# Kernel optimization log

Hardware: AMD Instinct MI355X
Metric: run time of the kernel (lower is better)

The kernel has to match this reference:

```python
import jax, jax.numpy as jnp
import numpy as np


def setup_inputs() -> dict:
    key = jax.random.key(0)
    ks = jax.random.split(key, 5)
    n, raw, d, h = 1024, 128, 128, 256
    s = lambda fan: 1.0 / np.sqrt(fan)
    return {
        "x": jax.random.normal(ks[0], (n, raw), jnp.float32),
        "W_enc": jax.random.normal(ks[1], (raw, d), jnp.float32) * s(raw),
        "b_enc": jnp.zeros((d,), jnp.float32),
        "W1": jax.random.normal(ks[2], (2 * d, h), jnp.float32) * s(2 * d),
        "b1": jnp.zeros((h,), jnp.float32),
        "W2": jax.random.normal(ks[3], (h, 1), jnp.float32) * s(h),
        "b2": jnp.zeros((1,), jnp.float32),
    }


def reference(x, W_enc, b_enc, W1, b1, W2, b2):
    # pathVAE.encode stand-in: linear projection to latent mean
    z = x @ W_enc + b_enc                      # [n, d]
    n, d = z.shape
    # Original builds feat[i, j] = concat(z[j], z[i]) of shape [n*n, 2d],
    # then Linear(2d->h). Split W1 so the quadratic concat is never built:
    # h[i, j] = z[j] @ W1[:d] + z[i] @ W1[d:] + b1
    A = z @ W1[:d]                             # acts on the "a" (j) half
    B = z @ W1[d:]                             # acts on the "b" (i) half
    hmat = A[None, :, :] + B[:, None, :] + b1  # [n, n, h]
    hmat = jax.nn.selu(hmat)
    o = hmat @ W2 + b2                         # [n, n, 1]
    o = jax.nn.hard_sigmoid(o)                 # relu6(x+3)/6, same as torch
    return o.reshape(n, n)
```

## Files before the change

### kernel.cpp

```cpp
#include <hip/hip_runtime.h>
#include <math.h>


#define LOG2E       1.4426950408889634f
#define SELU_AS     1.7580993408473766f
#define S_OVER_L2E  0.7282921587620419f

typedef float v2f __attribute__((ext_vector_type(2)));

__global__ __launch_bounds__(256) void prep_kernel(
    const float* __restrict__ x, const float* __restrict__ W_enc,
    const float* __restrict__ b_enc, const float* __restrict__ W1,
    const float* __restrict__ b1, const float* __restrict__ W2,
    const float* __restrict__ b2, float* __restrict__ PAI,
    float* __restrict__ PBI, float* __restrict__ basep)
{
    __shared__ float zs[512];
    int t = threadIdx.x, b = blockIdx.x;
    if (b < 256) {
        int r0 = b << 2;
        int r = t >> 6;
        int dd = (t & 63) << 1;
        const float* xr = x + (size_t)(r0 + r) * 128;
        v2f z = { b_enc[dd], b_enc[dd + 1] };
#pragma unroll 8
        for (int dl = 0; dl < 128; ++dl) {
            float xv = xr[dl];
            v2f xx = { xv, xv };
            v2f wv = *(const v2f*)(W_enc + (size_t)dl * 128 + dd);
            z = __builtin_elementwise_fma(xx, wv, z);
        }
        zs[r * 128 + dd] = z.x;
        zs[r * 128 + dd + 1] = z.y;
        __syncthreads();

        int c = t;
        float b1c = b1[c];
        float accA0 = 0.f, accA1 = 0.f, accA2 = 0.f, accA3 = 0.f;
        float accB0 = b1c, accB1 = b1c, accB2 = b1c, accB3 = b1c;
        const float* w1a = W1 + c;
        const float* w1b = W1 + 128 * 256 + c;
#pragma unroll 4
        for (int dl = 0; dl < 128; ++dl) {
            float wa = w1a[(size_t)dl * 256];
            float wb = w1b[(size_t)dl * 256];
            float z0 = zs[dl], z1 = zs[128 + dl], z2 = zs[256 + dl], z3 = zs[384 + dl];
            accA0 = fmaf(z0, wa, accA0); accB0 = fmaf(z0, wb, accB0);
            accA1 = fmaf(z1, wa, accA1); accB1 = fmaf(z1, wb, accB1);
            accA2 = fmaf(z2, wa, accA2); accB2 = fmaf(z2, wb, accB2);
            accA3 = fmaf(z3, wa, accA3); accB3 = fmaf(z3, wb, accB3);
        }
        float a0 = accA0 * LOG2E, a1 = accA1 * LOG2E;
        float a2 = accA2 * LOG2E, a3 = accA3 * LOG2E;
        float bb0 = accB0 * LOG2E, bb1 = accB1 * LOG2E;
        float bb2v = accB2 * LOG2E, bb3 = accB3 * LOG2E;
        float4 pa0, pa1, pb0, pb1;
        pa0.x = a0; pa0.y = a1;
        pa0.z = __builtin_amdgcn_exp2f(a0); pa0.w = __builtin_amdgcn_exp2f(a1);
        pa1.x = a2; pa1.y = a3;
        pa1.z = __builtin_amdgcn_exp2f(a2); pa1.w = __builtin_amdgcn_exp2f(a3);
        pb0.x = bb0; pb0.y = bb1;
        pb0.z = __builtin_amdgcn_exp2f(bb0); pb0.w = __builtin_amdgcn_exp2f(bb1);
        pb1.x = bb2v; pb1.y = bb3;
        pb1.z = __builtin_amdgcn_exp2f(bb2v); pb1.w = __builtin_amdgcn_exp2f(bb3);
        size_t o = (size_t)c * 2048 + (size_t)(r0 << 1);
        *(float4*)(PAI + o) = pa0;
        *(float4*)(PAI + o + 4) = pa1;
        *(float4*)(PBI + o) = pb0;
        *(float4*)(PBI + o + 4) = pb1;
    } else if (t < 64) {
        float s = W2[t] + W2[t + 64] + W2[t + 128] + W2[t + 192];
#pragma unroll
        for (int o = 32; o > 0; o >>= 1) s += __shfl_down(s, o);
        if (t == 0) basep[0] = fmaf(-SELU_AS, s, b2[0]);
    }
}

__global__ __launch_bounds__(256, 4) void pair_kernel(
    const float* __restrict__ PAI, const float* __restrict__ PBI,
    const float* __restrict__ W2, const float* __restrict__ basep,
    float* __restrict__ out)
{
    __shared__ __align__(16) float As[64 * 64];
    __shared__ __align__(16) float Bs[64 * 64];

    int t = threadIdx.x;
    int bj32 = blockIdx.x << 5, bi32 = blockIdx.y << 5;
    int jp = t & 15;
    int ip = t >> 4;

    v2f acc1[2] = {{0.f, 0.f}, {0.f, 0.f}};
    v2f acc2[2] = {{0.f, 0.f}, {0.f, 0.f}};
    const v2f vzero = {0.f, 0.f};
    const v2f vone  = {1.f, 1.f};

    for (int kc = 0; kc < 4; ++kc) {
        int k0 = kc << 6;
        if (kc) __syncthreads();
#pragma unroll
        for (int p = 0; p < 4; ++p) {
            int f = (p << 8) + t;
            int k_l = f >> 4;
            int col = (f & 15) << 2;
            size_t go = (size_t)(k0 + k_l) * 2048;
            *(float4*)&As[f << 2] = *(const float4*)(PAI + go + (bj32 << 1) + col);
            *(float4*)&Bs[f << 2] = *(const float4*)(PBI + go + (bi32 << 1) + col);
        }
        __syncthreads();

        const float* W2c = W2 + k0;
#pragma unroll 8
        for (int k = 0; k < 64; ++k) {
            float w = W2c[k];
            float4 av = *(const float4*)&As[(k << 6) + (jp << 2)];
            float4 bv = *(const float4*)&Bs[(k << 6) + (ip << 2)];
            v2f a01 = { av.x, av.y }, e01 = { av.z, av.w };
            v2f wv = { w, w };
#pragma unroll
            for (int i = 0; i < 2; ++i) {
                float bi = i ? bv.y : bv.x;
                float ei = i ? bv.w : bv.z;
                v2f bbv = { bi, bi };
                v2f eev = { ei, ei };
                v2f t01 = a01 + bbv;
                v2f p01 = e01 * eev;
                t01 = __builtin_elementwise_max(t01, vzero);
                p01 = __builtin_elementwise_min(p01, vone);
                acc1[i] = __builtin_elementwise_fma(wv, t01, acc1[i]);
                acc2[i] = __builtin_elementwise_fma(wv, p01, acc2[i]);
            }
        }
    }

    float base = basep[0];
    v2f basev = { base, base };
    v2f c1 = { S_OVER_L2E, S_OVER_L2E };
    v2f c2 = { SELU_AS, SELU_AS };
#pragma unroll
    for (int i = 0; i < 2; ++i) {
        v2f v = __builtin_elementwise_fma(c1, acc1[i],
                __builtin_elementwise_fma(c2, acc2[i], basev));
        float2 o;
        o.x = __saturatef(v.x * (1.0f / 6.0f) + 0.5f);
        o.y = __saturatef(v.y * (1.0f / 6.0f) + 0.5f);
        *(float2*)(out + (size_t)(bi32 + (ip << 1) + i) * 1024
                       + bj32 + (jp << 1)) = o;
    }
}

extern "C" void kernel_launch(void* const* d_in, const int* in_sizes, int n_in,
                              void* d_out, int out_size, void* d_ws, size_t ws_size,
                              hipStream_t stream) {
    const float* x     = (const float*)d_in[0];
    const float* W_enc = (const float*)d_in[1];
    const float* b_enc = (const float*)d_in[2];
    const float* W1    = (const float*)d_in[3];
    const float* b1    = (const float*)d_in[4];
    const float* W2    = (const float*)d_in[5];
    const float* b2    = (const float*)d_in[6];
    float* out = (float*)d_out;

    float* ws = (float*)d_ws;
    const int PLANE = 256 * 2048;
    float* PAI = ws;
    float* PBI = ws + PLANE;
    float* basep = ws + 2 * PLANE;

    prep_kernel<<<257, 256, 0, stream>>>(x, W_enc, b_enc, W1, b1, W2, b2,
                                         PAI, PBI, basep);
    pair_kernel<<<dim3(32, 32), 256, 0, stream>>>(PAI, PBI, W2, basep, out);
}
```

Baseline: 127.7 us.

## Use packed fp16 pair math with fdot2 and a larger 4x4 register tile

The prep kernel now stores the A/B projections and their exponentials as packed half2 values, with pairs of hidden units interleaved through lane shuffles. It also converts W2 to half2. The pair kernel computes add/max and mul/min in packed fp16 and accumulates with v_dot2 into fp32. Each thread now computes a 4x4 output tile over a 64x64 block instead of 2x2 over 32x32, which raises register reuse of the LDS loads. This roughly halves the ALU work per hidden unit, at the cost of fp16 precision for exp values and activations, which may overflow or lose accuracy.

```diff
diff --git a/kernel.cpp b/kernel.cpp
--- a/kernel.cpp
+++ b/kernel.cpp
@@ -7,13 +7,16 @@
 #define S_OVER_L2E  0.7282921587620419f
 
 typedef float v2f __attribute__((ext_vector_type(2)));
+typedef _Float16 v2h __attribute__((ext_vector_type(2)));
+typedef unsigned int u32;
 
 __global__ __launch_bounds__(256) void prep_kernel(
     const float* __restrict__ x, const float* __restrict__ W_enc,
     const float* __restrict__ b_enc, const float* __restrict__ W1,
     const float* __restrict__ b1, const float* __restrict__ W2,
-    const float* __restrict__ b2, float* __restrict__ PAI,
-    float* __restrict__ PBI, float* __restrict__ basep)
+    const float* __restrict__ b2, u32* __restrict__ PAa,
+    u32* __restrict__ PAe, u32* __restrict__ PBb, u32* __restrict__ PBe,
+    u32* __restrict__ W2h, float* __restrict__ basep)
 {
     __shared__ float zs[512];
     int t = threadIdx.x, b = blockIdx.x;
@@ -50,101 +53,129 @@
             accA2 = fmaf(z2, wa, accA2); accB2 = fmaf(z2, wb, accB2);
             accA3 = fmaf(z3, wa, accA3); accB3 = fmaf(z3, wb, accB3);
         }
-        float a0 = accA0 * LOG2E, a1 = accA1 * LOG2E;
-        float a2 = accA2 * LOG2E, a3 = accA3 * LOG2E;
-        float bb0 = accB0 * LOG2E, bb1 = accB1 * LOG2E;
-        float bb2v = accB2 * LOG2E, bb3 = accB3 * LOG2E;
-        float4 pa0, pa1, pb0, pb1;
-        pa0.x = a0; pa0.y = a1;
-        pa0.z = __builtin_amdgcn_exp2f(a0); pa0.w = __builtin_amdgcn_exp2f(a1);
-        pa1.x = a2; pa1.y = a3;
-        pa1.z = __builtin_amdgcn_exp2f(a2); pa1.w = __builtin_amdgcn_exp2f(a3);
-        pb0.x = bb0; pb0.y = bb1;
-        pb0.z = __builtin_amdgcn_exp2f(bb0); pb0.w = __builtin_amdgcn_exp2f(bb1);
-        pb1.x = bb2v; pb1.y = bb3;
-        pb1.z = __builtin_amdgcn_exp2f(bb2v); pb1.w = __builtin_amdgcn_exp2f(bb3);
-        size_t o = (size_t)c * 2048 + (size_t)(r0 << 1);
-        *(float4*)(PAI + o) = pa0;
-        *(float4*)(PAI + o + 4) = pa1;
-        *(float4*)(PBI + o) = pb0;
-        *(float4*)(PBI + o + 4) = pb1;
-    } else if (t < 64) {
-        float s = W2[t] + W2[t + 64] + W2[t + 128] + W2[t + 192];
-#pragma unroll
-        for (int o = 32; o > 0; o >>= 1) s += __shfl_down(s, o);
-        if (t == 0) basep[0] = fmaf(-SELU_AS, s, b2[0]);
+        float ar[4] = { accA0 * LOG2E, accA1 * LOG2E, accA2 * LOG2E, accA3 * LOG2E };
+        float br[4] = { accB0 * LOG2E, accB1 * LOG2E, accB2 * LOG2E, accB3 * LOG2E };
+        u32 pa[4], pe[4], pb[4], pf[4];
+        bool odd = (c & 1);
+#pragma unroll
+        for (int r2 = 0; r2 < 4; ++r2) {
+            float er = __builtin_amdgcn_exp2f(ar[r2]);
+            float fr = __builtin_amdgcn_exp2f(br[r2]);
+            float aN = __shfl_xor(ar[r2], 1);
+            float eN = __shfl_xor(er, 1);
+            float bN = __shfl_xor(br[r2], 1);
+            float fN = __shfl_xor(fr, 1);
+            pa[r2] = __builtin_bit_cast(u32, __builtin_amdgcn_cvt_pkrtz(ar[r2], aN));
+            pe[r2] = __builtin_bit_cast(u32, __builtin_amdgcn_cvt_pkrtz(er, eN));
+            pb[r2] = __builtin_bit_cast(u32, __builtin_amdgcn_cvt_pkrtz(bN, br[r2]));
+            pf[r2] = __builtin_bit_cast(u32, __builtin_amdgcn_cvt_pkrtz(fN, fr));
+        }
+        size_t o = (size_t)(c >> 1) * 1024 + r0;
+        if (!odd) {
+            *(uint4*)(PAa + o) = make_uint4(pa[0], pa[1], pa[2], pa[3]);
+            *(uint4*)(PAe + o) = make_uint4(pe[0], pe[1], pe[2], pe[3]);
+        } else {
+            *(uint4*)(PBb + o) = make_uint4(pb[0], pb[1], pb[2], pb[3]);
+            *(uint4*)(PBe + o) = make_uint4(pf[0], pf[1], pf[2], pf[3]);
+        }
+    } else {
+        if (t < 128) {
+            W2h[t] = __builtin_bit_cast(u32,
+                __builtin_amdgcn_cvt_pkrtz(W2[2 * t], W2[2 * t + 1]));
+        }
+        if (t < 64) {
+            float s = W2[t] + W2[t + 64] + W2[t + 128] + W2[t + 192];
+#pragma unroll
+            for (int o = 32; o > 0; o >>= 1) s += __shfl_down(s, o);
+            if (t == 0) basep[0] = fmaf(-SELU_AS, s, b2[0]);
+        }
     }
 }
 
-__global__ __launch_bounds__(256, 4) void pair_kernel(
-    const float* __restrict__ PAI, const float* __restrict__ PBI,
-    const float* __restrict__ W2, const float* __restrict__ basep,
+__global__ __launch_bounds__(256) void pair_kernel(
+    const u32* __restrict__ PAa, const u32* __restrict__ PAe,
+    const u32* __restrict__ PBb, const u32* __restrict__ PBe,
+    const u32* __restrict__ W2h, const float* __restrict__ basep,
     float* __restrict__ out)
 {
-    __shared__ __align__(16) float As[64 * 64];
-    __shared__ __align__(16) float Bs[64 * 64];
+    __shared__ __align__(16) u32 Aa[64 * 64];
+    __shared__ __align__(16) u32 Ae[64 * 64];
+    __shared__ __align__(16) u32 Bb[64 * 64];
+    __shared__ __align__(16) u32 Be[64 * 64];
 
     int t = threadIdx.x;
-    int bj32 = blockIdx.x << 5, bi32 = blockIdx.y << 5;
-    int jp = t & 15;
-    int ip = t >> 4;
-
-    v2f acc1[2] = {{0.f, 0.f}, {0.f, 0.f}};
-    v2f acc2[2] = {{0.f, 0.f}, {0.f, 0.f}};
-    const v2f vzero = {0.f, 0.f};
-    const v2f vone  = {1.f, 1.f};
-
-    for (int kc = 0; kc < 4; ++kc) {
-        int k0 = kc << 6;
-        if (kc) __syncthreads();
+    int bj64 = blockIdx.x << 6, bi64 = blockIdx.y << 6;
+    int tjx = t & 15, tiy = t >> 4;
+    int tj4 = tjx << 2, ti4 = tiy << 2;
+
+    float acc1[4][4], acc2[4][4];
+#pragma unroll
+    for (int i = 0; i < 4; ++i)
+#pragma unroll
+        for (int j = 0; j < 4; ++j) { acc1[i][j] = 0.f; acc2[i][j] = 0.f; }
+
+    const v2h hzero = { (_Float16)0.f, (_Float16)0.f };
+    const v2h hone  = { (_Float16)1.f, (_Float16)1.f };
+
+    for (int ch = 0; ch < 2; ++ch) {
+        if (ch) __syncthreads();
 #pragma unroll
         for (int p = 0; p < 4; ++p) {
-            int f = (p << 8) + t;
-            int k_l = f >> 4;
-            int col = (f & 15) << 2;
-            size_t go = (size_t)(k0 + k_l) * 2048;
-            *(float4*)&As[f << 2] = *(const float4*)(PAI + go + (bj32 << 1) + col);
-            *(float4*)&Bs[f << 2] = *(const float4*)(PBI + go + (bi32 << 1) + col);
+            int q = (p << 8) + t;
+            int k2l = q >> 4;
+            int jq = (q & 15) << 2;
+            size_t go = (size_t)((ch << 6) + k2l) * 1024;
+            *(uint4*)&Aa[q << 2] = *(const uint4*)(PAa + go + bj64 + jq);
+            *(uint4*)&Ae[q << 2] = *(const uint4*)(PAe + go + bj64 + jq);
+            *(uint4*)&Bb[q << 2] = *(const uint4*)(PBb + go + bi64 + jq);
+            *(uint4*)&Be[q << 2] = *(const uint4*)(PBe + go + bi64 + jq);
         }
         __syncthreads();
 
-        const float* W2c = W2 + k0;
-#pragma unroll 8
-        for (int k = 0; k < 64; ++k) {
-            float w = W2c[k];
-            float4 av = *(const float4*)&As[(k << 6) + (jp << 2)];
-            float4 bv = *(const float4*)&Bs[(k << 6) + (ip << 2)];
-            v2f a01 = { av.x, av.y }, e01 = { av.z, av.w };
-            v2f wv = { w, w };
-#pragma unroll
-            for (int i = 0; i < 2; ++i) {
-                float bi = i ? bv.y : bv.x;
-                float ei = i ? bv.w : bv.z;
-                v2f bbv = { bi, bi };
-                v2f eev = { ei, ei };
-                v2f t01 = a01 + bbv;
-                v2f p01 = e01 * eev;
-                t01 = __builtin_elementwise_max(t01, vzero);
-                p01 = __builtin_elementwise_min(p01, vone);
-                acc1[i] = __builtin_elementwise_fma(wv, t01, acc1[i]);
-                acc2[i] = __builtin_elementwise_fma(wv, p01, acc2[i]);
+        const u32* W2c = W2h + (ch << 6);
+#pragma unroll 4
+        for (int k2 = 0; k2 < 64; ++k2) {
+            v2h w2 = __builtin_bit_cast(v2h, W2c[k2]);
+            uint4 qa = *(const uint4*)&Aa[(k2 << 6) + tj4];
+            uint4 qe = *(const uint4*)&Ae[(k2 << 6) + tj4];
+            uint4 qb = *(const uint4*)&Bb[(k2 << 6) + ti4];
+            uint4 qf = *(const uint4*)&Be[(k2 << 6) + ti4];
+            v2h a[4] = { __builtin_bit_cast(v2h, qa.x), __builtin_bit_cast(v2h, qa.y),
+                         __builtin_bit_cast(v2h, qa.z), __builtin_bit_cast(v2h, qa.w) };
+            v2h e[4] = { __builtin_bit_cast(v2h, qe.x), __builtin_bit_cast(v2h, qe.y),
+                         __builtin_bit_cast(v2h, qe.z), __builtin_bit_cast(v2h, qe.w) };
+            v2h bb[4] = { __builtin_bit_cast(v2h, qb.x), __builtin_bit_cast(v2h, qb.y),
+                          __builtin_bit_cast(v2h, qb.z), __builtin_bit_cast(v2h, qb.w) };
+            v2h ff[4] = { __builtin_bit_cast(v2h, qf.x), __builtin_bit_cast(v2h, qf.y),
+                          __builtin_bit_cast(v2h, qf.z), __builtin_bit_cast(v2h, qf.w) };
+#pragma unroll
+            for (int i = 0; i < 4; ++i) {
+#pragma unroll
+                for (int j = 0; j < 4; ++j) {
+                    v2h t2 = a[j] + bb[i];
+                    v2h p2 = e[j] * ff[i];
+                    v2h m2 = __builtin_elementwise_max(t2, hzero);
+                    v2h n2 = __builtin_elementwise_min(p2, hone);
+                    acc1[i][j] = __builtin_amdgcn_fdot2(m2, w2, acc1[i][j], false);
+                    acc2[i][j] = __builtin_amdgcn_fdot2(n2, w2, acc2[i][j], false);
+                }
             }
         }
     }
 
     float base = basep[0];
-    v2f basev = { base, base };
-    v2f c1 = { S_OVER_L2E, S_OVER_L2E };
-    v2f c2 = { SELU_AS, SELU_AS };
-#pragma unroll
-    for (int i = 0; i < 2; ++i) {
-        v2f v = __builtin_elementwise_fma(c1, acc1[i],
-                __builtin_elementwise_fma(c2, acc2[i], basev));
-        float2 o;
-        o.x = __saturatef(v.x * (1.0f / 6.0f) + 0.5f);
-        o.y = __saturatef(v.y * (1.0f / 6.0f) + 0.5f);
-        *(float2*)(out + (size_t)(bi32 + (ip << 1) + i) * 1024
-                       + bj32 + (jp << 1)) = o;
+#pragma unroll
+    for (int i = 0; i < 4; ++i) {
+        float4 o;
+        float v0 = fmaf(S_OVER_L2E, acc1[i][0], fmaf(SELU_AS, acc2[i][0], base));
+        float v1 = fmaf(S_OVER_L2E, acc1[i][1], fmaf(SELU_AS, acc2[i][1], base));
+        float v2 = fmaf(S_OVER_L2E, acc1[i][2], fmaf(SELU_AS, acc2[i][2], base));
+        float v3 = fmaf(S_OVER_L2E, acc1[i][3], fmaf(SELU_AS, acc2[i][3], base));
+        o.x = __saturatef(v0 * (1.0f / 6.0f) + 0.5f);
+        o.y = __saturatef(v1 * (1.0f / 6.0f) + 0.5f);
+        o.z = __saturatef(v2 * (1.0f / 6.0f) + 0.5f);
+        o.w = __saturatef(v3 * (1.0f / 6.0f) + 0.5f);
+        *(float4*)(out + (size_t)(bi64 + ti4 + i) * 1024 + bj64 + tj4) = o;
     }
 }
 
@@ -160,13 +191,17 @@
     const float* b2    = (const float*)d_in[6];
     float* out = (float*)d_out;
 
-    float* ws = (float*)d_ws;
-    const int PLANE = 256 * 2048;
-    float* PAI = ws;
-    float* PBI = ws + PLANE;
-    float* basep = ws + 2 * PLANE;
+    u32* ws = (u32*)d_ws;
+    const int PLANE = 128 * 1024;
+    u32* PAa = ws;
+    u32* PAe = ws + PLANE;
+    u32* PBb = ws + 2 * PLANE;
+    u32* PBe = ws + 3 * PLANE;
+    u32* W2h = ws + 4 * PLANE;
+    float* basep = (float*)(ws + 4 * PLANE + 128);
 
     prep_kernel<<<257, 256, 0, stream>>>(x, W_enc, b_enc, W1, b1, W2, b2,
-                                         PAI, PBI, basep);
-    pair_kernel<<<dim3(32, 32), 256, 0, stream>>>(PAI, PBI, W2, basep, out);
+                                         PAa, PAe, PBb, PBe, W2h, basep);
+    pair_kernel<<<dim3(16, 16), 256, 0, stream>>>(PAa, PAe, PBb, PBe, W2h,
+                                                  basep, out);
 }
```

Result: faster. 116.5 us (-8.7%).
